# Optimization experiments

Measured on AMD Instinct MI355X. Metric: run time of the kernel, lower is better.

Reference implementation:

```python
import jax, jax.numpy as jnp
import numpy as np

NUM_EMBEDDINGS = 8192
EMBEDDING_DIM = 256
COMMITMENT_COST = 0.25
DECAY = 0.99
EPS = 1e-05


def setup_inputs() -> dict:
    key = jax.random.key(0)
    k1, k2, k3 = jax.random.split(key, 3)
    z = jax.random.normal(k1, (32, 1024, EMBEDDING_DIM), dtype=jnp.float32)
    embedding = jax.random.normal(k2, (NUM_EMBEDDINGS, EMBEDDING_DIM), dtype=jnp.float32)
    ema_cluster_size = jnp.zeros((NUM_EMBEDDINGS,), dtype=jnp.float32)
    ema_w = jax.random.normal(k3, (NUM_EMBEDDINGS, EMBEDDING_DIM), dtype=jnp.float32)
    return {"z": z, "embedding": embedding,
            "ema_cluster_size": ema_cluster_size, "ema_w": ema_w}


def reference(z, embedding, ema_cluster_size, ema_w):
    K, D = embedding.shape
    flat_z = z.reshape(-1, D)                                     # [N, D]

    # squared-distance matrix [N, K]: |z|^2 + |e|^2 - 2 z.e
    distances = (jnp.sum(flat_z * flat_z, axis=1, keepdims=True)
                 + jnp.sum(embedding * embedding, axis=1)
                 - 2.0 * flat_z @ embedding.T)
    indices = jnp.argmin(distances, axis=1)                       # [N] int

    # one-hot @ embedding == row gather
    z_q_flat = embedding[indices]                                 # [N, D]

    # --- training-mode EMA update (one-hot sums == scatter-adds) ---
    counts = jax.ops.segment_sum(jnp.ones_like(indices, dtype=flat_z.dtype),
                                 indices, num_segments=K)         # sum(encodings, 0)
    new_cluster_size = ema_cluster_size * DECAY + (1.0 - DECAY) * counts
    dw = jax.ops.segment_sum(flat_z, indices, num_segments=K)     # encodings.T @ flat_z
    new_ema_w = ema_w * DECAY + (1.0 - DECAY) * dw
    n = jnp.sum(new_cluster_size)
    cluster_size = (new_cluster_size + EPS) / (n + K * EPS) * n
    new_embedding = new_ema_w / cluster_size[:, None]

    # commitment loss uses z_q computed with the OLD embedding (detached)
    loss = COMMITMENT_COST * jnp.mean(
        (jax.lax.stop_gradient(z_q_flat) - flat_z) ** 2)
    # straight-through estimator
    z_q = flat_z + jax.lax.stop_gradient(z_q_flat - flat_z)
    z_q = z_q.reshape(z.shape)
    return z_q, loss, indices, new_embedding, new_cluster_size, new_ema_w
```

## Files before the change

### kernel.cpp

```cpp
#include <hip/hip_runtime.h>
#include <cfloat>

#define K_CODES 8192
#define DIM     256
#define NROWS   32768

#define O_ZQ    0
#define O_LOSS  8388608
#define O_IDX   8388609
#define O_NEMB  8421377
#define O_NCS   10518529
#define O_NEMAW 10526721

#define NCH          2
#define CODES_PER_CH (K_CODES / NCH)
#define NT_TILES     (CODES_PER_CH / 256)

typedef __attribute__((ext_vector_type(8))) short short8;
typedef __attribute__((ext_vector_type(4))) float floatx4;

__device__ __forceinline__ unsigned short f2bf_rne(float x) {
    unsigned u = __float_as_uint(x);
    u += 0x7fffu + ((u >> 16) & 1u);
    return (unsigned short)(u >> 16);
}
__device__ __forceinline__ float bf2f(unsigned short h) {
    return __uint_as_float(((unsigned)h) << 16);
}
__device__ __forceinline__ void async16(const void* g, void* l) {
    __builtin_amdgcn_global_load_lds(
        (const __attribute__((address_space(1))) void*)g,
        (__attribute__((address_space(3))) void*)l, 16, 0, 0);
}

__global__ void k_prep(const float* __restrict__ z, const float* __restrict__ emb,
                       unsigned short* __restrict__ zcat, unsigned short* __restrict__ ecat,
                       float* __restrict__ esq, int* __restrict__ zero16k) {
    const int b = blockIdx.x;
    if (b < 8192) {
        const int i = b * 256 + threadIdx.x;
        const int row = i >> 6;
        const int col = (i & 63) << 2;
        float4 v = ((const float4*)z)[i];
        float nx = -2.0f * v.x, ny = -2.0f * v.y, nz = -2.0f * v.z, nw = -2.0f * v.w;
        ushort4 h, l;
        h.x = f2bf_rne(nx); l.x = f2bf_rne(nx - bf2f(h.x));
        h.y = f2bf_rne(ny); l.y = f2bf_rne(ny - bf2f(h.y));
        h.z = f2bf_rne(nz); l.z = f2bf_rne(nz - bf2f(h.z));
        h.w = f2bf_rne(nw); l.w = f2bf_rne(nw - bf2f(h.w));
        *(ushort4*)&zcat[(size_t)row * 512 + col]       = h;
        *(ushort4*)&zcat[(size_t)row * 512 + 256 + col] = l;
    } else {
        const int gid  = (b - 8192) * 256 + threadIdx.x;
        if (gid < 2 * K_CODES) zero16k[gid] = 0;
        const int code = gid >> 6;
        const int lane = gid & 63;
        const int col  = lane << 2;
        float4 v = ((const float4*)emb)[code * 64 + lane];
        ushort4 h, l;
        h.x = f2bf_rne(v.x); l.x = f2bf_rne(v.x - bf2f(h.x));
        h.y = f2bf_rne(v.y); l.y = f2bf_rne(v.y - bf2f(h.y));
        h.z = f2bf_rne(v.z); l.z = f2bf_rne(v.z - bf2f(h.z));
        h.w = f2bf_rne(v.w); l.w = f2bf_rne(v.w - bf2f(h.w));
        *(ushort4*)&ecat[(size_t)code * 512 + col]       = h;
        *(ushort4*)&ecat[(size_t)code * 512 + 256 + col] = l;
        float s = fmaf(v.x, v.x, fmaf(v.y, v.y, fmaf(v.z, v.z, v.w * v.w)));
#pragma unroll
        for (int off = 32; off > 0; off >>= 1) s += __shfl_down(s, off, 64);
        if (lane == 0) esq[code] = s;
    }
}

__global__ __launch_bounds__(256, 2) void k_argmin_mfma(
        const unsigned short* __restrict__ zcat, const unsigned short* __restrict__ ecat,
        const float* __restrict__ esq,
        float* __restrict__ part_v, int* __restrict__ part_i) {
    __shared__ __align__(16) unsigned short a_s[128 * 64];
    __shared__ __align__(16) unsigned short b_s[256 * 64];
    const int t    = threadIdx.x;
    const int w    = t >> 6;
    const int lane = t & 63;
    const int quad = lane >> 4;
    const int m    = lane & 15;
    const int wrow = (w >> 1) * 64;
    const int wcol = (w & 1) * 128;
    const int row0   = blockIdx.x * 128;
    const int cbase0 = blockIdx.y * CODES_PER_CH;
    const int r8   = lane >> 3;
    const int cswz = ((lane & 7) ^ r8) * 8;
    const size_t aBase = (size_t)(row0 + r8) * 512 + cswz;
    const size_t bBase = (size_t)(cbase0 + r8) * 512 + cswz;
    const int mx  = m & 7;
    const int xo0 = ((0 + quad) ^ mx) * 8;
    const int xo1 = ((4 + quad) ^ mx) * 8;

    float    best_v[16];
    unsigned best_p[4];
#pragma unroll
    for (int r = 0; r < 16; ++r) best_v[r] = FLT_MAX;
#pragma unroll
    for (int i = 0; i < 4; ++i) best_p[i] = 0u;

    for (int nt = 0; nt < NT_TILES; ++nt) {
        const int cb = cbase0 + nt * 256;
        floatx4 acc[4][8];
#pragma unroll
        for (int j = 0; j < 8; ++j) {
            const float es = esq[cb + wcol + j * 16 + m];
#pragma unroll
            for (int i = 0; i < 4; ++i)
                acc[i][j] = (floatx4){es, es, es, es};
        }

        for (int k0 = 0; k0 < 768; k0 += 64) {
            const int off_a = (k0 & 255) | ((k0 & 512) >> 1);
            const int off_b = k0 & 511;
            __syncthreads();
            const int u0 = w * 12;
#pragma unroll
            for (int c = 0; c < 12; ++c) {
                const int u = u0 + c;
                if (u < 16) {
                    async16(zcat + aBase + (size_t)u * (8 * 512) + off_a, &a_s[u * 512]);
                } else {
                    const int q = u - 16;
                    async16(ecat + bBase + (size_t)(nt * 256 + q * 8) * 512 + off_b,
                            &b_s[q * 512]);
                }
            }
            __syncthreads();
#pragma unroll
            for (int half = 0; half < 2; ++half) {
                const int xo = half ? xo1 : xo0;
                short8 af[4], bfr[8];
#pragma unroll
                for (int i = 0; i < 4; ++i)
                    af[i] = *(const short8*)&a_s[(wrow + i * 16 + m) * 64 + xo];
#pragma unroll
                for (int j = 0; j < 8; ++j)
                    bfr[j] = *(const short8*)&b_s[(wcol + j * 16 + m) * 64 + xo];
#pragma unroll
                for (int i = 0; i < 4; ++i)
#pragma unroll
                    for (int j = 0; j < 8; ++j)
                        acc[i][j] = __builtin_amdgcn_mfma_f32_16x16x32_bf16(
                            af[i], bfr[j], acc[i][j], 0, 0, 0);
            }
        }
#pragma unroll
        for (int j = 0; j < 8; ++j) {
            const unsigned cand = (unsigned)(nt * 8 + j);
#pragma unroll
            for (int i = 0; i < 4; ++i)
#pragma unroll
                for (int reg = 0; reg < 4; ++reg) {
                    const float s = acc[i][j][reg];
                    const int r = i * 4 + reg;
                    if (s < best_v[r]) {
                        best_v[r] = s;
                        best_p[i] = (best_p[i] & ~(255u << (reg * 8))) | (cand << (reg * 8));
                    }
                }
        }
    }
    __syncthreads();
    float* redv = (float*)a_s;
    int*   redi = (int*)b_s;
#pragma unroll
    for (int i = 0; i < 4; ++i)
#pragma unroll
        for (int reg = 0; reg < 4; ++reg) {
            const int r = i * 4 + reg;
            const unsigned b = (best_p[i] >> (reg * 8)) & 255u;
            float v  = best_v[r];
            int   bi = cbase0 + (int)(b >> 3) * 256 + wcol + (int)(b & 7) * 16 + m;
#pragma unroll
            for (int off = 1; off < 16; off <<= 1) {
                const float ov = __shfl_xor(v, off, 64);
                const int   oi = __shfl_xor(bi, off, 64);
                if (ov < v || (ov == v && oi < bi)) { v = ov; bi = oi; }
            }
            if (m == 0) {
                const int row = wrow + i * 16 + quad * 4 + reg;
                redv[row * 2 + (w & 1)] = v;
                redi[row * 2 + (w & 1)] = bi;
            }
        }
    __syncthreads();
    if (t < 128) {
        const float v0 = redv[t * 2], v1 = redv[t * 2 + 1];
        const int   i0 = redi[t * 2], i1 = redi[t * 2 + 1];
        const bool  b1 = (v1 < v0) || (v1 == v0 && i1 < i0);
        const size_t o = (size_t)blockIdx.y * NROWS + blockIdx.x * 128 + t;
        part_v[o] = b1 ? v1 : v0;
        part_i[o] = b1 ? i1 : i0;
    }
}

__global__ void k_reduce_part(const float* __restrict__ pv, const int* __restrict__ pi,
                              int* __restrict__ idx_i, float* __restrict__ idx_f,
                              int* __restrict__ counts) {
    const int r = blockIdx.x * blockDim.x + threadIdx.x;
    float v = pv[r]; int bi = pi[r];
#pragma unroll
    for (int c = 1; c < NCH; ++c) {
        const float v2 = pv[(size_t)c * NROWS + r];
        const int   i2 = pi[(size_t)c * NROWS + r];
        if (v2 < v || (v2 == v && i2 < bi)) { v = v2; bi = i2; }
    }
    idx_i[r] = bi;
    idx_f[r] = (float)bi;
    atomicAdd(&counts[bi], 1);
}

__global__ void k_scan_ncs(const int* __restrict__ counts, const float* __restrict__ ema_cs,
                           int* __restrict__ offsets, float* __restrict__ ncs_out,
                           float* __restrict__ ntot) {
    __shared__ int   wsum[16];
    __shared__ float red[16];
    const int t = threadIdx.x;
    const int lane = t & 63, w = t >> 6;
    int c[8]; int s = 0; float fs = 0.0f;
#pragma unroll
    for (int u = 0; u < 8; ++u) {
        c[u] = counts[t * 8 + u]; s += c[u];
        const float v = fmaf(0.99f, ema_cs[t * 8 + u], 0.01f * (float)c[u]);
        ncs_out[t * 8 + u] = v;
        fs += v;
    }
    int inc = s;
#pragma unroll
    for (int off = 1; off < 64; off <<= 1) {
        const int n = __shfl_up(inc, off, 64);
        if (lane >= off) inc += n;
    }
#pragma unroll
    for (int off = 32; off > 0; off >>= 1) fs += __shfl_down(fs, off, 64);
    if (lane == 63) wsum[w] = inc;
    if (lane == 0)  red[w]  = fs;
    __syncthreads();
    if (t < 16) {
        int v = wsum[t];
#pragma unroll
        for (int off = 1; off < 16; off <<= 1) {
            const int n = __shfl_up(v, off, 64);
            if (t >= off) v += n;
        }
        wsum[t] = v;
        float fv = red[t];
#pragma unroll
        for (int off = 8; off > 0; off >>= 1) fv += __shfl_down(fv, off, 16);
        if (t == 0) *ntot = fv;
    }
    __syncthreads();
    int base = (w > 0 ? wsum[w - 1] : 0) + (inc - s);
#pragma unroll
    for (int u = 0; u < 8; ++u) { offsets[t * 8 + u] = base; base += c[u]; }
}

__global__ void k_zq(const float* __restrict__ z, const float* __restrict__ emb,
                     const int* __restrict__ idx_i, const int* __restrict__ offsets,
                     int* __restrict__ cursor, int* __restrict__ buckets,
                     float* __restrict__ zq, float* __restrict__ losspart) {
    __shared__ float lred[4];
    const int t = threadIdx.x;
    const int wr = t >> 6, lane = t & 63;
    const int row = blockIdx.x * 4 + wr;
    const int code = idx_i[row];
    float4 zv = ((const float4*)z)[row * 64 + lane];
    float4 ev = ((const float4*)emb)[(size_t)code * 64 + lane];
    float4 o = make_float4(zv.x + (ev.x - zv.x), zv.y + (ev.y - zv.y),
                           zv.z + (ev.z - zv.z), zv.w + (ev.w - zv.w));
    ((float4*)zq)[row * 64 + lane] = o;
    float dx = ev.x - zv.x, dy = ev.y - zv.y, dz = ev.z - zv.z, dw = ev.w - zv.w;
    float s = fmaf(dx, dx, fmaf(dy, dy, fmaf(dz, dz, dw * dw)));
#pragma unroll
    for (int off = 32; off > 0; off >>= 1) s += __shfl_down(s, off, 64);
    if (lane == 0) {
        lred[wr] = s;
        const int pos = atomicAdd(&cursor[code], 1);
        buckets[offsets[code] + pos] = row;
    }
    __syncthreads();
    if (t == 0) losspart[blockIdx.x] = (lred[0] + lred[1]) + (lred[2] + lred[3]);
}

__global__ void k_dw_nemb(const float* __restrict__ z, const float* __restrict__ ema_w,
                          const int* __restrict__ counts, const int* __restrict__ offsets,
                          const int* __restrict__ buckets, const float* __restrict__ ncs,
                          const float* __restrict__ ntot_p, const float* __restrict__ losspart,
                          float* __restrict__ nemaw, float* __restrict__ nemb,
                          float* __restrict__ loss_out) {
    __shared__ float lred[4];
    if (blockIdx.x == K_CODES) {
        const int t = threadIdx.x;
        float s = 0.0f;
        for (int i = t; i < 8192; i += 256) s += losspart[i];
#pragma unroll
        for (int off = 32; off > 0; off >>= 1) s += __shfl_down(s, off, 64);
        if ((t & 63) == 0) lred[t >> 6] = s;
        __syncthreads();
        if (t == 0)
            *loss_out = 0.25f * ((lred[0] + lred[1]) + (lred[2] + lred[3])) / 8388608.0f;
        return;
    }
    const int code = blockIdx.x;
    const int d    = threadIdx.x;
    const int cnt  = counts[code];
    const int off  = offsets[code];
    float acc = 0.0f;
    for (int it = 0; it < cnt; ++it)
        acc += z[(size_t)buckets[off + it] * DIM + d];
    const float wv = fmaf(0.99f, ema_w[(size_t)code * DIM + d], 0.01f * acc);
    nemaw[(size_t)code * DIM + d] = wv;
    const float n  = *ntot_p;
    const float cs = (ncs[code] + 1e-5f) * (n / (n + (float)K_CODES * 1e-5f));
    nemb[(size_t)code * DIM + d] = wv / cs;
}

#define BM   64
#define BN   128
#define LSTR 36

__global__ void k_esq_zero_fb(const float* __restrict__ emb, float* __restrict__ esq,
                              float* __restrict__ zbuf) {
    const int gid  = blockIdx.x * blockDim.x + threadIdx.x;
    if (gid < K_CODES + 2) zbuf[gid] = 0.0f;
    const int code = gid >> 6;
    const int lane = gid & 63;
    float4 v = ((const float4*)emb)[code * 64 + lane];
    float s = fmaf(v.x, v.x, fmaf(v.y, v.y, fmaf(v.z, v.z, v.w * v.w)));
#pragma unroll
    for (int off = 32; off > 0; off >>= 1) s += __shfl_down(s, off, 64);
    if (lane == 0) esq[code] = s;
}

__global__ void k_init_nemaw_fb(const float* __restrict__ ema_w, float* __restrict__ out) {
    const int i = blockIdx.x * blockDim.x + threadIdx.x;
    float4 v = ((const float4*)ema_w)[i];
    ((float4*)out)[i] = make_float4(0.99f * v.x, 0.99f * v.y, 0.99f * v.z, 0.99f * v.w);
}

__global__ __launch_bounds__(256, 2) void k_argmin_fb(
        const float* __restrict__ z, const float* __restrict__ emb,
        const float* __restrict__ esq, int* __restrict__ idx_i, float* __restrict__ idx_f) {
    __shared__ float z_s[BM * LSTR];
    __shared__ float e_s[BN * LSTR];
    const int t = threadIdx.x, tx = t & 15, ty = t >> 4;
    const int row0 = blockIdx.x * BM;
    float best[4]; int bidx[4];
#pragma unroll
    for (int r = 0; r < 4; ++r) { best[r] = FLT_MAX; bidx[r] = 0; }
    for (int k0 = 0; k0 < K_CODES; k0 += BN) {
        float acc[4][8];
#pragma unroll
        for (int r = 0; r < 4; ++r)
#pragma unroll
            for (int c = 0; c < 8; ++c) acc[r][c] = 0.0f;
        for (int d0 = 0; d0 < DIM; d0 += 32) {
            __syncthreads();
#pragma unroll
            for (int i = 0; i < 2; ++i) {
                int f = i * 256 + t, r = f >> 3, c4 = (f & 7) << 2;
                *(float4*)&z_s[r * LSTR + c4] =
                    *(const float4*)(z + (size_t)(row0 + r) * DIM + d0 + c4);
            }
#pragma unroll
            for (int i = 0; i < 4; ++i) {
                int f = i * 256 + t, c = f >> 3, c4 = (f & 7) << 2;
                *(float4*)&e_s[c * LSTR + c4] =
                    *(const float4*)(emb + (size_t)(k0 + c) * DIM + d0 + c4);
            }
            __syncthreads();
#pragma unroll
            for (int dd = 0; dd < 32; dd += 4) {
                float4 a[4], b[8];
#pragma unroll
                for (int j = 0; j < 4; ++j)
                    a[j] = *(const float4*)&z_s[(ty * 4 + j) * LSTR + dd];
#pragma unroll
                for (int j = 0; j < 8; ++j)
                    b[j] = *(const float4*)&e_s[(tx + 16 * j) * LSTR + dd];
#pragma unroll
                for (int r = 0; r < 4; ++r)
#pragma unroll
                    for (int c = 0; c < 8; ++c) {
                        acc[r][c] = fmaf(a[r].x, b[c].x, acc[r][c]);
                        acc[r][c] = fmaf(a[r].y, b[c].y, acc[r][c]);
                        acc[r][c] = fmaf(a[r].z, b[c].z, acc[r][c]);
                        acc[r][c] = fmaf(a[r].w, b[c].w, acc[r][c]);
                    }
            }
        }
#pragma unroll
        for (int c = 0; c < 8; ++c) {
            const int code = k0 + tx + 16 * c;
            const float es = esq[code];
#pragma unroll
            for (int r = 0; r < 4; ++r) {
                float s = fmaf(-2.0f, acc[r][c], es);
                if (s < best[r] || (s == best[r] && code < bidx[r])) {
                    best[r] = s; bidx[r] = code;
                }
            }
        }
    }
    __syncthreads();
    float* rv = e_s; int* ri = (int*)z_s;
#pragma unroll
    for (int r = 0; r < 4; ++r) {
        rv[(ty * 4 + r) * 16 + tx] = best[r];
        ri[(ty * 4 + r) * 16 + tx] = bidx[r];
    }
    __syncthreads();
    if (t < 64) {
        float mv = rv[t * 16]; int mi = ri[t * 16];
#pragma unroll
        for (int i = 1; i < 16; ++i) {
            float v = rv[t * 16 + i]; int vi = ri[t * 16 + i];
            if (v < mv || (v == mv && vi < mi)) { mv = v; mi = vi; }
        }
        idx_i[row0 + t] = mi;
        idx_f[row0 + t] = (float)mi;
    }
}

__global__ void k_gather_fb(const float* __restrict__ z, const float* __restrict__ emb,
                            const int* __restrict__ idx_i, float* __restrict__ zq,
                            float* __restrict__ nemaw, float* __restrict__ counts,
                            float* __restrict__ loss) {
    const int gid  = blockIdx.x * blockDim.x + threadIdx.x;
    const int row  = gid >> 6;
    const int lane = gid & 63;
    const int code = idx_i[row];
    float4 zv = ((const float4*)z)[row * 64 + lane];
    float4 ev = ((const float4*)emb)[(size_t)code * 64 + lane];
    float4 o = make_float4(zv.x + (ev.x - zv.x), zv.y + (ev.y - zv.y),
                           zv.z + (ev.z - zv.z), zv.w + (ev.w - zv.w));
    ((float4*)zq)[row * 64 + lane] = o;
    float dx = ev.x - zv.x, dy = ev.y - zv.y, dz = ev.z - zv.z, dw = ev.w - zv.w;
    float s = fmaf(dx, dx, fmaf(dy, dy, fmaf(dz, dz, dw * dw)));
#pragma unroll
    for (int off = 32; off > 0; off >>= 1) s += __shfl_down(s, off, 64);
    if (lane == 0) { atomicAdd(loss, s); atomicAdd(&counts[code], 1.0f); }
    float* base = nemaw + (size_t)code * DIM + lane * 4;
    atomicAdd(base + 0, 0.01f * zv.x);
    atomicAdd(base + 1, 0.01f * zv.y);
    atomicAdd(base + 2, 0.01f * zv.z);
    atomicAdd(base + 3, 0.01f * zv.w);
}

__global__ void k_ncs_fb(const float* __restrict__ ema_cs, const float* __restrict__ counts,
                         float* __restrict__ ncs_out, float* __restrict__ ntot,
                         const float* __restrict__ loss_in, float* __restrict__ loss_out) {
    __shared__ float red[16];
    const int t = threadIdx.x;
    float s = 0.0f;
    for (int i = t; i < K_CODES; i += 1024) {
        float v = fmaf(0.99f, ema_cs[i], 0.01f * counts[i]);
        ncs_out[i] = v; s += v;
    }
#pragma unroll
    for (int off = 32; off > 0; off >>= 1) s += __shfl_down(s, off, 64);
    if ((t & 63) == 0) red[t >> 6] = s;
    __syncthreads();
    if (t < 16) {
        float v = red[t];
#pragma unroll
        for (int off = 8; off > 0; off >>= 1) v += __shfl_down(v, off, 16);
        if (t == 0) { *ntot = v; *loss_out = 0.25f * (*loss_in) / 8388608.0f; }
    }
}

__global__ void k_nemb_fb(const float* __restrict__ nemaw, const float* __restrict__ ncs,
                          const float* __restrict__ ntot_p, float* __restrict__ nemb) {
    const int i4 = blockIdx.x * blockDim.x + threadIdx.x;
    const int k  = i4 >> 6;
    const float n   = *ntot_p;
    const float inv = n / (n + (float)K_CODES * 1e-5f);
    const float cs  = (ncs[k] + 1e-5f) * inv;
    float4 wv = ((const float4*)nemaw)[i4];
    ((float4*)nemb)[i4] = make_float4(wv.x / cs, wv.y / cs, wv.z / cs, wv.w / cs);
}

extern "C" void kernel_launch(void* const* d_in, const int* in_sizes, int n_in,
                              void* d_out, int out_size, void* d_ws, size_t ws_size,
                              hipStream_t stream) {
    const float* z      = (const float*)d_in[0];
    const float* emb    = (const float*)d_in[1];
    const float* ema_cs = (const float*)d_in[2];
    const float* ema_w  = (const float*)d_in[3];
    float* out = (float*)d_out;
    char* wsb = (char*)d_ws;

    unsigned short* zcat    = (unsigned short*)wsb;
    unsigned short* ecat    = (unsigned short*)(wsb + 33554432);
    float*          part_v  = (float*)(wsb + 41943040);
    int*            part_i  = (int*)  (wsb + 42467328);
    float*          esq     = (float*)(wsb + 42991616);
    int*            ws_idx  = (int*)  (wsb + 43024384);
    int*            counts  = (int*)  (wsb + 43155456);
    int*            cursor  = (int*)  (wsb + 43188224);
    int*            offsets = (int*)  (wsb + 43220992);
    int*            buckets = (int*)  (wsb + 43253760);
    float*          lpart   = (float*)(wsb + 43384832);
    float*          ws_loss = (float*)(wsb + 43417600);
    float*          ws_ntot = ws_loss + 1;

    if (ws_size >= (size_t)43417616) {
        k_prep       <<<10240, 256, 0, stream>>>(z, emb, zcat, ecat, esq, counts);
        k_argmin_mfma<<<dim3(NROWS / 128, NCH), 256, 0, stream>>>(
            zcat, ecat, esq, part_v, part_i);
        k_reduce_part<<<NROWS / 256, 256, 0, stream>>>(part_v, part_i, ws_idx,
                                                       out + O_IDX, counts);
        k_scan_ncs   <<<1, 1024, 0, stream>>>(counts, ema_cs, offsets,
                                              out + O_NCS, ws_ntot);
        k_zq         <<<NROWS / 4, 256, 0, stream>>>(z, emb, ws_idx, offsets, cursor,
                                                     buckets, out + O_ZQ, lpart);
        k_dw_nemb    <<<K_CODES + 1, 256, 0, stream>>>(z, ema_w, counts, offsets, buckets,
                                                       out + O_NCS, ws_ntot, lpart,
                                                       out + O_NEMAW, out + O_NEMB,
                                                       out + O_LOSS);
    } else {
        int*   f_idx    = (int*)wsb;
        float* f_counts = (float*)(wsb + 131072);
        float* f_loss   = f_counts + K_CODES;
        float* f_ntot   = f_loss + 1;
        float* f_esq    = (float*)(wsb + 163856);
        k_esq_zero_fb  <<<2048, 256, 0, stream>>>(emb, f_esq, f_counts);
        k_init_nemaw_fb<<<2048, 256, 0, stream>>>(ema_w, out + O_NEMAW);
        k_argmin_fb    <<<NROWS / BM, 256, 0, stream>>>(z, emb, f_esq, f_idx, out + O_IDX);
        k_gather_fb    <<<NROWS / 4, 256, 0, stream>>>(z, emb, f_idx, out + O_ZQ,
                                                       out + O_NEMAW, f_counts, f_loss);
        k_ncs_fb       <<<1, 1024, 0, stream>>>(ema_cs, f_counts, out + O_NCS, f_ntot,
                                                f_loss, out + O_LOSS);
        k_nemb_fb      <<<2048, 256, 0, stream>>>(out + O_NEMAW, out + O_NCS, f_ntot,
                                                  out + O_NEMB);
    }
}
```

Baseline: 639.7 us.

## Double-buffer LDS tiles in argmin MFMA kernel to overlap loads with compute

Replaces the single 64-wide K-step LDS staging (two syncs per step) with two 32-wide ping-pong buffers. The async global-to-LDS copy of the next K slice is issued before the MFMA compute on the current one, leaving one barrier per half-step. It also prefetches the next tile's codebook norms into registers and changes the swizzle for the narrower rows. LDS use stays the same, but the loop now has more barriers in total, and the smaller K chunk per sync may limit how much latency is hidden.

Measured after the change: 787.2 us. +23.1%, slower.

```diff
diff --git a/kernel.cpp b/kernel.cpp
--- a/kernel.cpp
+++ b/kernel.cpp
@@ -71,12 +71,45 @@
     }
 }
 
+#define STAGE(AS, BS, ntv, offa, offb)                                          \
+    do {                                                                        \
+        _Pragma("unroll")                                                       \
+        for (int c_ = 0; c_ < 6; ++c_) {                                        \
+            const int u_ = w * 6 + c_;                                          \
+            if (u_ < 8)                                                         \
+                async16(aGlob + (size_t)u_ * 8192 + (offa), &AS[u_ * 512]);     \
+            else                                                                \
+                async16(bGlob + (size_t)(ntv) * 131072 +                        \
+                            (size_t)(u_ - 8) * 8192 + (offb),                   \
+                        &BS[(u_ - 8) * 512]);                                   \
+        }                                                                       \
+    } while (0)
+
+#define COMPUTE(AS, BS)                                                         \
+    do {                                                                        \
+        short8 af_[4], bf_[8];                                                  \
+        _Pragma("unroll")                                                       \
+        for (int i_ = 0; i_ < 4; ++i_)                                          \
+            af_[i_] = *(const short8*)&AS[(wrow + i_ * 16 + m) * 32 + xo];      \
+        _Pragma("unroll")                                                       \
+        for (int j_ = 0; j_ < 8; ++j_)                                          \
+            bf_[j_] = *(const short8*)&BS[(wcol + j_ * 16 + m) * 32 + xo];      \
+        _Pragma("unroll")                                                       \
+        for (int i_ = 0; i_ < 4; ++i_)                                          \
+            _Pragma("unroll")                                                   \
+            for (int j_ = 0; j_ < 8; ++j_)                                      \
+                acc[i_][j_] = __builtin_amdgcn_mfma_f32_16x16x32_bf16(          \
+                    af_[i_], bf_[j_], acc[i_][j_], 0, 0, 0);                    \
+    } while (0)
+
 __global__ __launch_bounds__(256, 2) void k_argmin_mfma(
         const unsigned short* __restrict__ zcat, const unsigned short* __restrict__ ecat,
         const float* __restrict__ esq,
         float* __restrict__ part_v, int* __restrict__ part_i) {
-    __shared__ __align__(16) unsigned short a_s[128 * 64];
-    __shared__ __align__(16) unsigned short b_s[256 * 64];
+    __shared__ __align__(16) unsigned short a0_s[128 * 32];
+    __shared__ __align__(16) unsigned short a1_s[128 * 32];
+    __shared__ __align__(16) unsigned short b0_s[256 * 32];
+    __shared__ __align__(16) unsigned short b1_s[256 * 32];
     const int t    = threadIdx.x;
     const int w    = t >> 6;
     const int lane = t & 63;
@@ -86,13 +119,13 @@
     const int wcol = (w & 1) * 128;
     const int row0   = blockIdx.x * 128;
     const int cbase0 = blockIdx.y * CODES_PER_CH;
-    const int r8   = lane >> 3;
-    const int cswz = ((lane & 7) ^ r8) * 8;
-    const size_t aBase = (size_t)(row0 + r8) * 512 + cswz;
-    const size_t bBase = (size_t)(cbase0 + r8) * 512 + cswz;
-    const int mx  = m & 7;
-    const int xo0 = ((0 + quad) ^ mx) * 8;
-    const int xo1 = ((4 + quad) ^ mx) * 8;
+
+    const int    swz    = (((lane & 3) ^ ((lane >> 3) & 3)) << 3);
+    const size_t srcrow = (size_t)(lane >> 2) * 512 + swz;
+    const unsigned short* aGlob = zcat + (size_t)row0 * 512 + srcrow;
+    const unsigned short* bGlob = ecat + (size_t)cbase0 * 512 + srcrow;
+
+    const int xo = ((quad ^ ((m >> 1) & 3)) << 3);
 
     float    best_v[16];
     unsigned best_p[4];
@@ -101,50 +134,42 @@
 #pragma unroll
     for (int i = 0; i < 4; ++i) best_p[i] = 0u;
 
+    STAGE(a0_s, b0_s, 0, 0, 0);
+    float es[8];
+#pragma unroll
+    for (int j = 0; j < 8; ++j) es[j] = esq[cbase0 + wcol + j * 16 + m];
+    __syncthreads();
+
     for (int nt = 0; nt < NT_TILES; ++nt) {
-        const int cb = cbase0 + nt * 256;
         floatx4 acc[4][8];
 #pragma unroll
         for (int j = 0; j < 8; ++j) {
-            const float es = esq[cb + wcol + j * 16 + m];
-#pragma unroll
-            for (int i = 0; i < 4; ++i)
-                acc[i][j] = (floatx4){es, es, es, es};
-        }
-
-        for (int k0 = 0; k0 < 768; k0 += 64) {
-            const int off_a = (k0 & 255) | ((k0 & 512) >> 1);
-            const int off_b = k0 & 511;
-            __syncthreads();
-            const int u0 = w * 12;
-#pragma unroll
-            for (int c = 0; c < 12; ++c) {
-                const int u = u0 + c;
-                if (u < 16) {
-                    async16(zcat + aBase + (size_t)u * (8 * 512) + off_a, &a_s[u * 512]);
-                } else {
-                    const int q = u - 16;
-                    async16(ecat + bBase + (size_t)(nt * 256 + q * 8) * 512 + off_b,
-                            &b_s[q * 512]);
+            const float e = es[j];
+#pragma unroll
+            for (int i = 0; i < 4; ++i) acc[i][j] = (floatx4){e, e, e, e};
+        }
+
+        for (int kk2 = 0; kk2 < 12; ++kk2) {
+            {
+                const int nk0 = kk2 * 64 + 32;
+                STAGE(a1_s, b1_s, nt, (nk0 & 255) | ((nk0 & 512) >> 1), nk0 & 511);
+                COMPUTE(a0_s, b0_s);
+                __syncthreads();
+            }
+            {
+                if (kk2 < 11) {
+                    const int nk0 = kk2 * 64 + 64;
+                    STAGE(a0_s, b0_s, nt, (nk0 & 255) | ((nk0 & 512) >> 1), nk0 & 511);
+                } else if (nt + 1 < NT_TILES) {
+                    STAGE(a0_s, b0_s, nt + 1, 0, 0);
                 }
-            }
-            __syncthreads();
-#pragma unroll
-            for (int half = 0; half < 2; ++half) {
-                const int xo = half ? xo1 : xo0;
-                short8 af[4], bfr[8];
-#pragma unroll
-                for (int i = 0; i < 4; ++i)
-                    af[i] = *(const short8*)&a_s[(wrow + i * 16 + m) * 64 + xo];
-#pragma unroll
-                for (int j = 0; j < 8; ++j)
-                    bfr[j] = *(const short8*)&b_s[(wcol + j * 16 + m) * 64 + xo];
-#pragma unroll
-                for (int i = 0; i < 4; ++i)
+                if (kk2 == 10 && nt + 1 < NT_TILES) {
 #pragma unroll
                     for (int j = 0; j < 8; ++j)
-                        acc[i][j] = __builtin_amdgcn_mfma_f32_16x16x32_bf16(
-                            af[i], bfr[j], acc[i][j], 0, 0, 0);
+                        es[j] = esq[cbase0 + (nt + 1) * 256 + wcol + j * 16 + m];
+                }
+                COMPUTE(a1_s, b1_s);
+                __syncthreads();
             }
         }
 #pragma unroll
@@ -164,8 +189,8 @@
         }
     }
     __syncthreads();
-    float* redv = (float*)a_s;
-    int*   redi = (int*)b_s;
+    float* redv = (float*)a0_s;
+    int*   redi = (int*)b0_s;
 #pragma unroll
     for (int i = 0; i < 4; ++i)
 #pragma unroll
@@ -196,6 +221,9 @@
         part_i[o] = b1 ? i1 : i0;
     }
 }
+
+#undef STAGE
+#undef COMPUTE
 
 __global__ void k_reduce_part(const float* __restrict__ pv, const int* __restrict__ pi,
                               int* __restrict__ idx_i, float* __restrict__ idx_f,
```

## Restructure argmin MFMA kernel into 256x256 tiles with 4-stage async LDS pipeline

Applied to the files above, without the earlier changes.

The distance/argmin GEMM kernel now uses 512-thread blocks covering 256 rows by 256 codes, with a 4-deep ring of async global-to-LDS buffers (128 KB dynamic LDS) and explicit vmcnt waits instead of a load-then-sync per k-step. LDS reads use inline ds_read_b128 with a new swizzle, the MFMA bursts are raised in priority, and the esq loads are prefetched one tile ahead. The aim is to hide global load latency behind MFMA work and to increase operand reuse per block. In exchange it needs more LDS and registers per block (32 running minima per thread), which may reduce occupancy, and the hand-counted waitcnt and barrier scheme is fragile.

Result: slower. 655.6 us (+2.5%).

```diff
diff --git a/kernel.cpp b/kernel.cpp
--- a/kernel.cpp
+++ b/kernel.cpp
@@ -15,6 +15,9 @@
 #define NCH          2
 #define CODES_PER_CH (K_CODES / NCH)
 #define NT_TILES     (CODES_PER_CH / 256)
+#define KT_PER_NT    24
+#define KT_TOTAL     (NT_TILES * KT_PER_NT)
+#define LDS_BYTES    131072
 
 typedef __attribute__((ext_vector_type(8))) short short8;
 typedef __attribute__((ext_vector_type(4))) float floatx4;
@@ -32,6 +35,12 @@
         (const __attribute__((address_space(1))) void*)g,
         (__attribute__((address_space(3))) void*)l, 16, 0, 0);
 }
+__device__ __forceinline__ unsigned ldsaddr(const void* p) {
+    return (unsigned)(unsigned long long)
+        (const __attribute__((address_space(3))) void*)p;
+}
+#define DSR(dst, addr, off)                                                     \
+    asm volatile("ds_read_b128 %0, %1 offset:" #off : "=v"(dst) : "v"(addr))
 
 __global__ void k_prep(const float* __restrict__ z, const float* __restrict__ emb,
                        unsigned short* __restrict__ zcat, unsigned short* __restrict__ ecat,
@@ -71,87 +80,132 @@
     }
 }
 
-__global__ __launch_bounds__(256, 2) void k_argmin_mfma(
+__global__ __launch_bounds__(512, 2) void k_argmin_mfma(
         const unsigned short* __restrict__ zcat, const unsigned short* __restrict__ ecat,
         const float* __restrict__ esq,
         float* __restrict__ part_v, int* __restrict__ part_i) {
-    __shared__ __align__(16) unsigned short a_s[128 * 64];
-    __shared__ __align__(16) unsigned short b_s[256 * 64];
+    extern __shared__ __align__(16) unsigned short s_all[];
     const int t    = threadIdx.x;
     const int w    = t >> 6;
     const int lane = t & 63;
     const int quad = lane >> 4;
     const int m    = lane & 15;
-    const int wrow = (w >> 1) * 64;
-    const int wcol = (w & 1) * 128;
-    const int row0   = blockIdx.x * 128;
+    const int wr   = w >> 2;
+    const int wc   = w & 3;
+    const int row0   = blockIdx.x * 256;
     const int cbase0 = blockIdx.y * CODES_PER_CH;
-    const int r8   = lane >> 3;
-    const int cswz = ((lane & 7) ^ r8) * 8;
-    const size_t aBase = (size_t)(row0 + r8) * 512 + cswz;
-    const size_t bBase = (size_t)(cbase0 + r8) * 512 + cswz;
-    const int mx  = m & 7;
-    const int xo0 = ((0 + quad) ^ mx) * 8;
-    const int xo1 = ((4 + quad) ^ mx) * 8;
-
-    float    best_v[16];
-    unsigned best_p[4];
-#pragma unroll
-    for (int r = 0; r < 16; ++r) best_v[r] = FLT_MAX;
-#pragma unroll
-    for (int i = 0; i < 4; ++i) best_p[i] = 0u;
+
+    const int prow = t >> 2;
+    const int pch  = t & 3;
+    const int lc   = pch ^ ((prow >> 1) & 3);
+    const unsigned short* aSrc = zcat + (size_t)(row0 + prow) * 512 + lc * 8;
+    const unsigned short* bSrc = ecat + (size_t)(cbase0 + prow) * 512 + lc * 8;
+    const int dstU = prow * 32 + pch * 8;
+
+    const int xo2 = (quad ^ ((m >> 1) & 3)) << 4;
+    const unsigned lb = ldsaddr(s_all);
+    const unsigned aRdTB = lb + (unsigned)((wr * 128 + m) * 64 + xo2);
+    const unsigned bRdTB = lb + 16384u + (unsigned)((wc * 64 + m) * 64 + xo2);
+
+    float    best_v[32];
+    unsigned best_p[8];
+#pragma unroll
+    for (int r = 0; r < 32; ++r) best_v[r] = FLT_MAX;
+#pragma unroll
+    for (int i = 0; i < 8; ++i) best_p[i] = 0u;
+
+#pragma unroll
+    for (int G = 0; G < 3; ++G) {
+        const int k0   = G * 32;
+        const int offA = (k0 & 255) | ((k0 & 512) >> 1);
+        const int offB = k0 & 511;
+        unsigned short* dA = s_all + G * 16384 + dstU;
+        async16(aSrc + offA, dA);
+        async16(aSrc + 65536 + offA, dA + 4096);
+        async16(bSrc + offB, dA + 8192);
+        async16(bSrc + 65536 + offB, dA + 12288);
+    }
+    float es[4];
+#pragma unroll
+    for (int j = 0; j < 4; ++j) es[j] = esq[cbase0 + wc * 64 + j * 16 + m];
 
     for (int nt = 0; nt < NT_TILES; ++nt) {
-        const int cb = cbase0 + nt * 256;
-        floatx4 acc[4][8];
-#pragma unroll
-        for (int j = 0; j < 8; ++j) {
-            const float es = esq[cb + wcol + j * 16 + m];
+        floatx4 acc[8][4];
+#pragma unroll
+        for (int j = 0; j < 4; ++j) {
+            const float e = es[j];
+#pragma unroll
+            for (int i = 0; i < 8; ++i) acc[i][j] = (floatx4){e, e, e, e};
+        }
+
+#pragma unroll 1
+        for (int kk = 0; kk < KT_PER_NT; ++kk) {
+            const int g = nt * KT_PER_NT + kk;
+            if (g < KT_TOTAL - 2)
+                asm volatile("s_waitcnt vmcnt(8)" ::: "memory");
+            else if (g == KT_TOTAL - 2)
+                asm volatile("s_waitcnt vmcnt(4)" ::: "memory");
+            else
+                asm volatile("s_waitcnt vmcnt(0)" ::: "memory");
+            __builtin_amdgcn_s_barrier();
+
+            const int G = g + 3;
+            const unsigned short* sA = aSrc;
+            const unsigned short* sB = bSrc;
+            unsigned short* dD = s_all;
+            if (G < KT_TOTAL) {
+                const int ntS = G / KT_PER_NT;
+                const int k0  = (G - ntS * KT_PER_NT) * 32;
+                sA = aSrc + ((k0 & 255) | ((k0 & 512) >> 1));
+                sB = bSrc + (size_t)ntS * 131072 + (k0 & 511);
+                dD = s_all + (G & 3) * 16384 + dstU;
+            }
+            const unsigned bub   = (unsigned)((g & 3) << 15);
+            const unsigned addrA = aRdTB + bub;
+            const unsigned addrB = bRdTB + bub;
+
+            short8 af[4], bf[4];
+            DSR(bf[0], addrB, 0);    DSR(bf[1], addrB, 1024);
+            DSR(bf[2], addrB, 2048); DSR(bf[3], addrB, 3072);
+            DSR(af[0], addrA, 0);    DSR(af[1], addrA, 1024);
+            DSR(af[2], addrA, 2048); DSR(af[3], addrA, 3072);
+            if (G < KT_TOTAL) {
+                async16(sA, dD);
+                async16(sA + 65536, dD + 4096);
+            }
+            asm volatile("s_waitcnt lgkmcnt(0)" ::: "memory");
+            __builtin_amdgcn_sched_barrier(0);
+            __builtin_amdgcn_s_setprio(1);
 #pragma unroll
             for (int i = 0; i < 4; ++i)
-                acc[i][j] = (floatx4){es, es, es, es};
-        }
-
-        for (int k0 = 0; k0 < 768; k0 += 64) {
-            const int off_a = (k0 & 255) | ((k0 & 512) >> 1);
-            const int off_b = k0 & 511;
-            __syncthreads();
-            const int u0 = w * 12;
-#pragma unroll
-            for (int c = 0; c < 12; ++c) {
-                const int u = u0 + c;
-                if (u < 16) {
-                    async16(zcat + aBase + (size_t)u * (8 * 512) + off_a, &a_s[u * 512]);
-                } else {
-                    const int q = u - 16;
-                    async16(ecat + bBase + (size_t)(nt * 256 + q * 8) * 512 + off_b,
-                            &b_s[q * 512]);
-                }
-            }
-            __syncthreads();
-#pragma unroll
-            for (int half = 0; half < 2; ++half) {
-                const int xo = half ? xo1 : xo0;
-                short8 af[4], bfr[8];
-#pragma unroll
-                for (int i = 0; i < 4; ++i)
-                    af[i] = *(const short8*)&a_s[(wrow + i * 16 + m) * 64 + xo];
-#pragma unroll
-                for (int j = 0; j < 8; ++j)
-                    bfr[j] = *(const short8*)&b_s[(wcol + j * 16 + m) * 64 + xo];
-#pragma unroll
-                for (int i = 0; i < 4; ++i)
-#pragma unroll
-                    for (int j = 0; j < 8; ++j)
-                        acc[i][j] = __builtin_amdgcn_mfma_f32_16x16x32_bf16(
-                            af[i], bfr[j], acc[i][j], 0, 0, 0);
-            }
-        }
-#pragma unroll
-        for (int j = 0; j < 8; ++j) {
-            const unsigned cand = (unsigned)(nt * 8 + j);
+#pragma unroll
+                for (int j = 0; j < 4; ++j)
+                    acc[i][j] = __builtin_amdgcn_mfma_f32_16x16x32_bf16(
+                        af[i], bf[j], acc[i][j], 0, 0, 0);
+            __builtin_amdgcn_s_setprio(0);
+            __builtin_amdgcn_s_barrier();
+            DSR(af[0], addrA, 4096); DSR(af[1], addrA, 5120);
+            DSR(af[2], addrA, 6144); DSR(af[3], addrA, 7168);
+            if (G < KT_TOTAL) {
+                async16(sB, dD + 8192);
+                async16(sB + 65536, dD + 12288);
+            }
+            asm volatile("s_waitcnt lgkmcnt(0)" ::: "memory");
+            __builtin_amdgcn_sched_barrier(0);
+            __builtin_amdgcn_s_setprio(1);
 #pragma unroll
             for (int i = 0; i < 4; ++i)
+#pragma unroll
+                for (int j = 0; j < 4; ++j)
+                    acc[4 + i][j] = __builtin_amdgcn_mfma_f32_16x16x32_bf16(
+                        af[i], bf[j], acc[4 + i][j], 0, 0, 0);
+            __builtin_amdgcn_s_setprio(0);
+        }
+#pragma unroll
+        for (int j = 0; j < 4; ++j) {
+            const unsigned cand = (unsigned)(nt * 4 + j);
+#pragma unroll
+            for (int i = 0; i < 8; ++i)
 #pragma unroll
                 for (int reg = 0; reg < 4; ++reg) {
                     const float s = acc[i][j][reg];
@@ -162,18 +216,23 @@
                     }
                 }
         }
-    }
-    __syncthreads();
-    float* redv = (float*)a_s;
-    int*   redi = (int*)b_s;
-#pragma unroll
-    for (int i = 0; i < 4; ++i)
+        if (nt + 1 < NT_TILES) {
+#pragma unroll
+            for (int j = 0; j < 4; ++j)
+                es[j] = esq[cbase0 + (nt + 1) * 256 + wc * 64 + j * 16 + m];
+        }
+    }
+    __syncthreads();
+    float* redv = (float*)s_all;
+    int*   redi = (int*)(s_all + 2048);
+#pragma unroll
+    for (int i = 0; i < 8; ++i)
 #pragma unroll
         for (int reg = 0; reg < 4; ++reg) {
             const int r = i * 4 + reg;
             const unsigned b = (best_p[i] >> (reg * 8)) & 255u;
             float v  = best_v[r];
-            int   bi = cbase0 + (int)(b >> 3) * 256 + wcol + (int)(b & 7) * 16 + m;
+            int   bi = cbase0 + (int)(b >> 2) * 256 + wc * 64 + (int)(b & 3) * 16 + m;
 #pragma unroll
             for (int off = 1; off < 16; off <<= 1) {
                 const float ov = __shfl_xor(v, off, 64);
@@ -181,19 +240,23 @@
                 if (ov < v || (ov == v && oi < bi)) { v = ov; bi = oi; }
             }
             if (m == 0) {
-                const int row = wrow + i * 16 + quad * 4 + reg;
-                redv[row * 2 + (w & 1)] = v;
-                redi[row * 2 + (w & 1)] = bi;
-            }
-        }
-    __syncthreads();
-    if (t < 128) {
-        const float v0 = redv[t * 2], v1 = redv[t * 2 + 1];
-        const int   i0 = redi[t * 2], i1 = redi[t * 2 + 1];
-        const bool  b1 = (v1 < v0) || (v1 == v0 && i1 < i0);
-        const size_t o = (size_t)blockIdx.y * NROWS + blockIdx.x * 128 + t;
-        part_v[o] = b1 ? v1 : v0;
-        part_i[o] = b1 ? i1 : i0;
+                const int rl = wr * 128 + i * 16 + quad * 4 + reg;
+                redv[rl * 4 + wc] = v;
+                redi[rl * 4 + wc] = bi;
+            }
+        }
+    __syncthreads();
+    if (t < 256) {
+        float v = redv[t * 4]; int bi = redi[t * 4];
+#pragma unroll
+        for (int c = 1; c < 4; ++c) {
+            const float v2 = redv[t * 4 + c];
+            const int   i2 = redi[t * 4 + c];
+            if (v2 < v || (v2 == v && i2 < bi)) { v = v2; bi = i2; }
+        }
+        const size_t o = (size_t)blockIdx.y * NROWS + blockIdx.x * 256 + t;
+        part_v[o] = v;
+        part_i[o] = bi;
     }
 }
 
@@ -508,8 +571,15 @@
     float*          ws_ntot = ws_loss + 1;
 
     if (ws_size >= (size_t)43417616) {
+        static bool lds_attr_set = false;
+        if (!lds_attr_set) {
+            (void)hipFuncSetAttribute((const void*)k_argmin_mfma,
+                                      hipFuncAttributeMaxDynamicSharedMemorySize,
+                                      LDS_BYTES);
+            lds_attr_set = true;
+        }
         k_prep       <<<10240, 256, 0, stream>>>(z, emb, zcat, ecat, esq, counts);
-        k_argmin_mfma<<<dim3(NROWS / 128, NCH), 256, 0, stream>>>(
+        k_argmin_mfma<<<dim3(NROWS / 256, NCH), 512, LDS_BYTES, stream>>>(
             zcat, ecat, esq, part_v, part_i);
         k_reduce_part<<<NROWS / 256, 256, 0, stream>>>(part_v, part_i, ws_idx,
                                                        out + O_IDX, counts);
```
